# Kernel optimization log

Hardware: AMD Instinct MI355X
Metric: run time of the kernel (lower is better)

The kernel has to match this reference:

```python
import jax, jax.numpy as jnp
import numpy as np

N, DIM, EMB = 8192, 128, 16
WIDTHS = [64, 32, 16]


def setup_inputs() -> dict:
    key = jax.random.key(0)
    ks = jax.random.split(key, 16)
    x = jax.random.normal(ks[0], (N, DIM), dtype=jnp.float32)
    dims = [DIM] + WIDTHS + [EMB]  # 128 -> 64 -> 32 -> 16 -> 16
    params = {}
    for i in range(4):
        fan_in, fan_out = dims[i], dims[i + 1]
        params[f"W{i+1}"] = jax.random.normal(ks[1 + 2 * i], (fan_in, fan_out), dtype=jnp.float32) * (1.0 / np.sqrt(fan_in))
        params[f"b{i+1}"] = jax.random.normal(ks[2 + 2 * i], (fan_out,), dtype=jnp.float32) * 0.01
    return {"x": x, **params}


def _encode(x, W1, b1, W2, b2, W3, b3, W4, b4):
    h = jax.nn.relu(x @ W1 + b1)
    h = jax.nn.relu(h @ W2 + b2)
    h = jax.nn.relu(h @ W3 + b3)
    return h @ W4 + b4  # [N, EMB]


def _tstudent_probs(z):
    # squared euclidean distances via the norm trick (avoids [N,N,EMB] tensor)
    sq = jnp.sum(z * z, axis=1)  # [N]
    dist = jnp.maximum(sq[:, None] + sq[None, :] - 2.0 * (z @ z.T), 0.0)  # [N,N]
    numerator = 1.0 / (1.0 + dist)
    return numerator / jnp.sum(numerator, axis=1, keepdims=True)


def reference(x, W1, b1, W2, b2, W3, b3, W4, b4):
    z = _encode(x, W1, b1, W2, b2, W3, b3, W4, b4)
    return _tstudent_probs(z)
```

## Files before the change

kernel.cpp:

```cpp
#include <hip/hip_runtime.h>

#define N 8192
#define DIM 128
#define NCHUNK 32

typedef float f32x4 __attribute__((ext_vector_type(4)));

__global__ __launch_bounds__(64) void encoder_kernel(
    const float* __restrict__ x,
    const float* __restrict__ W1, const float* __restrict__ b1,
    const float* __restrict__ W2, const float* __restrict__ b2,
    const float* __restrict__ W3, const float* __restrict__ b3,
    const float* __restrict__ W4, const float* __restrict__ b4,
    float* __restrict__ z, float* __restrict__ zT, float* __restrict__ sqout)
{
    __shared__ float sW2[64 * 32];
    __shared__ float sW3[32 * 16];
    __shared__ float sW4[16 * 16];
    __shared__ float sb1[64];
    __shared__ float sb2[32];
    __shared__ float sb3[16];
    __shared__ float sb4[16];
    __shared__ float sW1[128 * 64];
    __shared__ float sh1[64 * 65];

    int t = threadIdx.x;
    float* sh2 = sW1;
    float* sh3 = sW1 + 2112;

    for (int idx = t; idx < 128 * 64; idx += 64) sW1[idx] = W1[idx];
    for (int idx = t; idx < 64 * 32; idx += 64) sW2[idx] = W2[idx];
    for (int idx = t; idx < 32 * 16; idx += 64) sW3[idx] = W3[idx];
    for (int idx = t; idx < 16 * 16; idx += 64) sW4[idx] = W4[idx];
    sb1[t] = b1[t];
    if (t < 32) sb2[t] = b2[t];
    if (t < 16) { sb3[t] = b3[t]; sb4[t] = b4[t]; }
    __syncthreads();

    int row = blockIdx.x * 64 + t;
    const float4* xr = (const float4*)(x + (size_t)row * DIM);

    float h1[64];
    #pragma unroll
    for (int k = 0; k < 64; ++k) h1[k] = sb1[k];
    for (int j4 = 0; j4 < 32; ++j4) {
        float4 xv = xr[j4];
        const float* w0 = &sW1[(j4 * 4 + 0) * 64];
        const float* w1 = &sW1[(j4 * 4 + 1) * 64];
        const float* w2 = &sW1[(j4 * 4 + 2) * 64];
        const float* w3 = &sW1[(j4 * 4 + 3) * 64];
        #pragma unroll
        for (int k = 0; k < 64; ++k) h1[k] = fmaf(xv.x, w0[k], h1[k]);
        #pragma unroll
        for (int k = 0; k < 64; ++k) h1[k] = fmaf(xv.y, w1[k], h1[k]);
        #pragma unroll
        for (int k = 0; k < 64; ++k) h1[k] = fmaf(xv.z, w2[k], h1[k]);
        #pragma unroll
        for (int k = 0; k < 64; ++k) h1[k] = fmaf(xv.w, w3[k], h1[k]);
    }
    #pragma unroll
    for (int k = 0; k < 64; ++k) sh1[t * 65 + k] = fmaxf(h1[k], 0.0f);

    float h2[32];
    #pragma unroll
    for (int k = 0; k < 32; ++k) h2[k] = sb2[k];
    for (int j = 0; j < 64; ++j) {
        float a = sh1[t * 65 + j];
        #pragma unroll
        for (int k = 0; k < 32; ++k) h2[k] = fmaf(a, sW2[j * 32 + k], h2[k]);
    }
    #pragma unroll
    for (int k = 0; k < 32; ++k) sh2[t * 33 + k] = fmaxf(h2[k], 0.0f);

    float h3[16];
    #pragma unroll
    for (int k = 0; k < 16; ++k) h3[k] = sb3[k];
    for (int j = 0; j < 32; ++j) {
        float a = sh2[t * 33 + j];
        #pragma unroll
        for (int k = 0; k < 16; ++k) h3[k] = fmaf(a, sW3[j * 16 + k], h3[k]);
    }
    #pragma unroll
    for (int k = 0; k < 16; ++k) sh3[t * 17 + k] = fmaxf(h3[k], 0.0f);

    float zo[16];
    #pragma unroll
    for (int k = 0; k < 16; ++k) zo[k] = sb4[k];
    for (int j = 0; j < 16; ++j) {
        float a = sh3[t * 17 + j];
        #pragma unroll
        for (int k = 0; k < 16; ++k) zo[k] = fmaf(a, sW4[j * 16 + k], zo[k]);
    }

    float s = 0.0f;
    #pragma unroll
    for (int k = 0; k < 16; ++k) s = fmaf(zo[k], zo[k], s);
    sqout[row] = s;
    float4* zr = (float4*)(z + (size_t)row * 16);
    zr[0] = make_float4(zo[0], zo[1], zo[2], zo[3]);
    zr[1] = make_float4(zo[4], zo[5], zo[6], zo[7]);
    zr[2] = make_float4(zo[8], zo[9], zo[10], zo[11]);
    zr[3] = make_float4(zo[12], zo[13], zo[14], zo[15]);
    #pragma unroll
    for (int k = 0; k < 16; ++k) zT[(size_t)k * N + row] = zo[k];
}

__global__ __launch_bounds__(256) void pass1_kernel(
    const float* __restrict__ z, const float* __restrict__ sq,
    float* __restrict__ partial)
{
    __shared__ float s_zj[256 * 16];
    __shared__ float s_sqj[256];

    int t = threadIdx.x;
    int i0 = blockIdx.x * 256 + t;
    int i1 = i0 + 4096;
    int jb = blockIdx.y * 256;

    {
        const float4* src = (const float4*)(z + (size_t)(jb + t) * 16);
        float4* dst = (float4*)(s_zj + t * 16);
        dst[0] = src[0]; dst[1] = src[1]; dst[2] = src[2]; dst[3] = src[3];
        s_sqj[t] = sq[jb + t];
    }

    float zi0[16], zi1[16];
    {
        const float4* p0 = (const float4*)(z + (size_t)i0 * 16);
        const float4* p1 = (const float4*)(z + (size_t)i1 * 16);
        #pragma unroll
        for (int q = 0; q < 4; ++q) {
            float4 v0 = p0[q]; float4 v1 = p1[q];
            zi0[4*q] = v0.x; zi0[4*q+1] = v0.y; zi0[4*q+2] = v0.z; zi0[4*q+3] = v0.w;
            zi1[4*q] = v1.x; zi1[4*q+1] = v1.y; zi1[4*q+2] = v1.z; zi1[4*q+3] = v1.w;
        }
    }
    float sqi0 = sq[i0], sqi1 = sq[i1];
    __syncthreads();

    float acc0 = 0.0f, acc1 = 0.0f;
    #pragma unroll 4
    for (int jj = 0; jj < 256; ++jj) {
        const float* zj = s_zj + jj * 16;
        float d0 = 0.0f, d1 = 0.0f;
        #pragma unroll
        for (int k = 0; k < 16; ++k) {
            float w = zj[k];
            d0 = fmaf(zi0[k], w, d0);
            d1 = fmaf(zi1[k], w, d1);
        }
        float sj = s_sqj[jj];
        float dist0 = fmaxf(fmaf(-2.0f, d0, sqi0 + sj), 0.0f);
        float dist1 = fmaxf(fmaf(-2.0f, d1, sqi1 + sj), 0.0f);
        acc0 += __builtin_amdgcn_rcpf(1.0f + dist0);
        acc1 += __builtin_amdgcn_rcpf(1.0f + dist1);
    }
    partial[blockIdx.y * N + i0] = acc0;
    partial[blockIdx.y * N + i1] = acc1;
}

__global__ __launch_bounds__(256) void pass2_kernel(
    const float* __restrict__ z, const float* __restrict__ zT,
    const float* __restrict__ sq,
    const float* __restrict__ partial, float* __restrict__ out)
{
    __shared__ float s_inv[4];

    int t = threadIdx.x;
    int ibase = blockIdx.x * 4;
    int w = t >> 6, lane = t & 63;

    {
        float v = (lane < NCHUNK) ? partial[(size_t)lane * N + ibase + w] : 0.0f;
        #pragma unroll
        for (int off = 32; off > 0; off >>= 1) v += __shfl_xor(v, off, 64);
        if (lane == 0) s_inv[w] = 1.0f / v;
    }

    float zi[4][16];
    float sqi[4];
    #pragma unroll
    for (int rr = 0; rr < 4; ++rr) {
        const float4* p = (const float4*)(z + (size_t)(ibase + rr) * 16);
        #pragma unroll
        for (int q = 0; q < 4; ++q) {
            float4 v = p[q];
            zi[rr][4*q]   = v.x; zi[rr][4*q+1] = v.y;
            zi[rr][4*q+2] = v.z; zi[rr][4*q+3] = v.w;
        }
        sqi[rr] = sq[ibase + rr];
    }
    __syncthreads();
    float inv[4];
    #pragma unroll
    for (int rr = 0; rr < 4; ++rr) inv[rr] = s_inv[rr];

    for (int jb = 0; jb < N; jb += 1024) {
        int j0 = jb + t * 4;
        f32x4 zjT[16];
        #pragma unroll
        for (int k = 0; k < 16; ++k)
            zjT[k] = *(const f32x4*)(zT + (size_t)k * N + j0);
        f32x4 sqj = *(const f32x4*)(sq + j0);

        #pragma unroll
        for (int rr = 0; rr < 4; ++rr) {
            f32x4 d = {0.0f, 0.0f, 0.0f, 0.0f};
            #pragma unroll
            for (int k = 0; k < 16; ++k) d += zi[rr][k] * zjT[k];
            f32x4 dist = sqi[rr] + sqj - 2.0f * d;
            f32x4 num;
            num.x = __builtin_amdgcn_rcpf(1.0f + fmaxf(dist.x, 0.0f)) * inv[rr];
            num.y = __builtin_amdgcn_rcpf(1.0f + fmaxf(dist.y, 0.0f)) * inv[rr];
            num.z = __builtin_amdgcn_rcpf(1.0f + fmaxf(dist.z, 0.0f)) * inv[rr];
            num.w = __builtin_amdgcn_rcpf(1.0f + fmaxf(dist.w, 0.0f)) * inv[rr];
            __builtin_nontemporal_store(num,
                (f32x4*)(out + (size_t)(ibase + rr) * N + j0));
        }
    }
}

extern "C" void kernel_launch(void* const* d_in, const int* in_sizes, int n_in,
                              void* d_out, int out_size, void* d_ws, size_t ws_size,
                              hipStream_t stream) {
    const float* x  = (const float*)d_in[0];
    const float* W1 = (const float*)d_in[1];
    const float* b1 = (const float*)d_in[2];
    const float* W2 = (const float*)d_in[3];
    const float* b2 = (const float*)d_in[4];
    const float* W3 = (const float*)d_in[5];
    const float* b3 = (const float*)d_in[6];
    const float* W4 = (const float*)d_in[7];
    const float* b4 = (const float*)d_in[8];
    float* out = (float*)d_out;

    float* ws = (float*)d_ws;
    float* z       = ws;
    float* zT      = ws + N * 16;
    float* sqv     = ws + N * 32;
    float* partial = ws + N * 32 + N;

    encoder_kernel<<<128, 64, 0, stream>>>(x, W1, b1, W2, b2, W3, b3, W4, b4, z, zT, sqv);
    pass1_kernel<<<dim3(16, NCHUNK), 256, 0, stream>>>(z, sqv, partial);
    pass2_kernel<<<N / 4, 256, 0, stream>>>(z, zT, sqv, partial, out);
}
```

Before: 376.9 us.

## Restructure row-sum pass to mirror pass2 layout with in-block full reduction

The row-sum pass is rewritten so that each block owns 4 rows and sweeps all N columns, reading z transposed from global memory with vector loads. It then reduces across warps in shared memory and writes the inverse row sum directly. This removes the 32-chunk partial buffer, the shared-memory staging of z_j, and the extra reduction at the start of pass2. In exchange the pass launches 2048 blocks with 4 rows each, which gives more parallelism, but each block rereads the whole zT and sq arrays.

After: 389.3 us. +3.3%, slower.

```diff
diff --git a/kernel.cpp b/kernel.cpp
--- a/kernel.cpp
+++ b/kernel.cpp
@@ -2,7 +2,6 @@
 
 #define N 8192
 #define DIM 128
-#define NCHUNK 32
 
 typedef float f32x4 __attribute__((ext_vector_type(4)));
 
@@ -106,76 +105,76 @@
 }
 
 __global__ __launch_bounds__(256) void pass1_kernel(
-    const float* __restrict__ z, const float* __restrict__ sq,
-    float* __restrict__ partial)
+    const float* __restrict__ z, const float* __restrict__ zT,
+    const float* __restrict__ sq, float* __restrict__ rowinv)
 {
-    __shared__ float s_zj[256 * 16];
-    __shared__ float s_sqj[256];
+    __shared__ float s_part[4][4];
 
     int t = threadIdx.x;
-    int i0 = blockIdx.x * 256 + t;
-    int i1 = i0 + 4096;
-    int jb = blockIdx.y * 256;
-
-    {
-        const float4* src = (const float4*)(z + (size_t)(jb + t) * 16);
-        float4* dst = (float4*)(s_zj + t * 16);
-        dst[0] = src[0]; dst[1] = src[1]; dst[2] = src[2]; dst[3] = src[3];
-        s_sqj[t] = sq[jb + t];
-    }
-
-    float zi0[16], zi1[16];
-    {
-        const float4* p0 = (const float4*)(z + (size_t)i0 * 16);
-        const float4* p1 = (const float4*)(z + (size_t)i1 * 16);
+    int ibase = blockIdx.x * 4;
+    int w = t >> 6, lane = t & 63;
+
+    float zi[4][16];
+    float sqi[4];
+    #pragma unroll
+    for (int rr = 0; rr < 4; ++rr) {
+        const float4* p = (const float4*)(z + (size_t)(ibase + rr) * 16);
         #pragma unroll
         for (int q = 0; q < 4; ++q) {
-            float4 v0 = p0[q]; float4 v1 = p1[q];
-            zi0[4*q] = v0.x; zi0[4*q+1] = v0.y; zi0[4*q+2] = v0.z; zi0[4*q+3] = v0.w;
-            zi1[4*q] = v1.x; zi1[4*q+1] = v1.y; zi1[4*q+2] = v1.z; zi1[4*q+3] = v1.w;
-        }
-    }
-    float sqi0 = sq[i0], sqi1 = sq[i1];
+            float4 v = p[q];
+            zi[rr][4*q]   = v.x; zi[rr][4*q+1] = v.y;
+            zi[rr][4*q+2] = v.z; zi[rr][4*q+3] = v.w;
+        }
+        sqi[rr] = sq[ibase + rr];
+    }
+
+    float acc[4] = {0.0f, 0.0f, 0.0f, 0.0f};
+    for (int jb = 0; jb < N; jb += 1024) {
+        int j0 = jb + t * 4;
+        f32x4 zjT[16];
+        #pragma unroll
+        for (int k = 0; k < 16; ++k)
+            zjT[k] = *(const f32x4*)(zT + (size_t)k * N + j0);
+        f32x4 sqj = *(const f32x4*)(sq + j0);
+
+        #pragma unroll
+        for (int rr = 0; rr < 4; ++rr) {
+            f32x4 d = {0.0f, 0.0f, 0.0f, 0.0f};
+            #pragma unroll
+            for (int k = 0; k < 16; ++k) d += zi[rr][k] * zjT[k];
+            f32x4 dist = sqi[rr] + sqj - 2.0f * d;
+            acc[rr] += __builtin_amdgcn_rcpf(1.0f + fmaxf(dist.x, 0.0f))
+                     + __builtin_amdgcn_rcpf(1.0f + fmaxf(dist.y, 0.0f))
+                     + __builtin_amdgcn_rcpf(1.0f + fmaxf(dist.z, 0.0f))
+                     + __builtin_amdgcn_rcpf(1.0f + fmaxf(dist.w, 0.0f));
+        }
+    }
+
+    #pragma unroll
+    for (int rr = 0; rr < 4; ++rr) {
+        float v = acc[rr];
+        #pragma unroll
+        for (int off = 32; off > 0; off >>= 1) v += __shfl_xor(v, off, 64);
+        if (lane == 0) s_part[w][rr] = v;
+    }
     __syncthreads();
-
-    float acc0 = 0.0f, acc1 = 0.0f;
-    #pragma unroll 4
-    for (int jj = 0; jj < 256; ++jj) {
-        const float* zj = s_zj + jj * 16;
-        float d0 = 0.0f, d1 = 0.0f;
-        #pragma unroll
-        for (int k = 0; k < 16; ++k) {
-            float w = zj[k];
-            d0 = fmaf(zi0[k], w, d0);
-            d1 = fmaf(zi1[k], w, d1);
-        }
-        float sj = s_sqj[jj];
-        float dist0 = fmaxf(fmaf(-2.0f, d0, sqi0 + sj), 0.0f);
-        float dist1 = fmaxf(fmaf(-2.0f, d1, sqi1 + sj), 0.0f);
-        acc0 += __builtin_amdgcn_rcpf(1.0f + dist0);
-        acc1 += __builtin_amdgcn_rcpf(1.0f + dist1);
-    }
-    partial[blockIdx.y * N + i0] = acc0;
-    partial[blockIdx.y * N + i1] = acc1;
+    if (t < 4) {
+        float s = s_part[0][t] + s_part[1][t] + s_part[2][t] + s_part[3][t];
+        rowinv[ibase + t] = 1.0f / s;
+    }
 }
 
 __global__ __launch_bounds__(256) void pass2_kernel(
     const float* __restrict__ z, const float* __restrict__ zT,
     const float* __restrict__ sq,
-    const float* __restrict__ partial, float* __restrict__ out)
+    const float* __restrict__ rowinv, float* __restrict__ out)
 {
     __shared__ float s_inv[4];
 
     int t = threadIdx.x;
     int ibase = blockIdx.x * 4;
-    int w = t >> 6, lane = t & 63;
-
-    {
-        float v = (lane < NCHUNK) ? partial[(size_t)lane * N + ibase + w] : 0.0f;
-        #pragma unroll
-        for (int off = 32; off > 0; off >>= 1) v += __shfl_xor(v, off, 64);
-        if (lane == 0) s_inv[w] = 1.0f / v;
-    }
+
+    if (t < 4) s_inv[t] = rowinv[ibase + t];
 
     float zi[4][16];
     float sqi[4];
@@ -235,12 +234,12 @@
     float* out = (float*)d_out;
 
     float* ws = (float*)d_ws;
-    float* z       = ws;
-    float* zT      = ws + N * 16;
-    float* sqv     = ws + N * 32;
-    float* partial = ws + N * 32 + N;
+    float* z      = ws;
+    float* zT     = ws + N * 16;
+    float* sqv    = ws + N * 32;
+    float* rowinv = ws + N * 32 + N;
 
     encoder_kernel<<<128, 64, 0, stream>>>(x, W1, b1, W2, b2, W3, b3, W4, b4, z, zT, sqv);
-    pass1_kernel<<<dim3(16, NCHUNK), 256, 0, stream>>>(z, sqv, partial);
-    pass2_kernel<<<N / 4, 256, 0, stream>>>(z, zT, sqv, partial, out);
-}
+    pass1_kernel<<<N / 4, 256, 0, stream>>>(z, zT, sqv, rowinv);
+    pass2_kernel<<<N / 4, 256, 0, stream>>>(z, zT, sqv, rowinv, out);
+}
```
